# Optimization experiments

Measured on AMD Instinct MI355X. Metric: run time of the kernel, lower is better.

Reference implementation:

```python
import jax, jax.numpy as jnp
import numpy as np

L, D, H, KV, HD, FF, V = 2, 2048, 16, 8, 128, 6144, 32000
B, T = 1, 2048
THETA = 1.0e6
EPS = 1e-6
NEG = -1e30


def _rope_tables():
    inv = 1.0 / (THETA ** (np.arange(0, HD, 2, dtype=np.float32) / HD))
    ang = np.arange(T, dtype=np.float32)[:, None] * inv[None, :]
    ang = np.concatenate([ang, ang], axis=1)  # [T, HD]
    return jnp.asarray(np.cos(ang), jnp.float32), jnp.asarray(np.sin(ang), jnp.float32)


def _rmsnorm(x, scale):
    v = jnp.mean(x * x, axis=-1, keepdims=True)
    return x * jax.lax.rsqrt(v + EPS) * scale


def _rope(x, cos, sin):
    # x: [B, h, T, HD]; rotate-half RoPE with full-dim cos/sin tables
    x1, x2 = x[..., : HD // 2], x[..., HD // 2 :]
    rot = jnp.concatenate([-x2, x1], axis=-1)
    return x * cos[None, None] + rot * sin[None, None]


def setup_inputs() -> dict:
    key = jax.random.key(0)
    ks = jax.random.split(key, 12)
    s = 0.02
    return {
        "token_ids": jax.random.randint(ks[0], (B, T), 0, V),
        "emb": jax.random.normal(ks[1], (V, D), jnp.float32) * s,
        "Wq": jax.random.normal(ks[2], (L, D, H * HD), jnp.float32) * s,
        "Wk": jax.random.normal(ks[3], (L, D, KV * HD), jnp.float32) * s,
        "Wv": jax.random.normal(ks[4], (L, D, KV * HD), jnp.float32) * s,
        "Wo": jax.random.normal(ks[5], (L, H * HD, D), jnp.float32) * s,
        "qn": jnp.ones((L, HD), jnp.float32),
        "kn": jnp.ones((L, HD), jnp.float32),
        "W1": jax.random.normal(ks[6], (L, D, FF), jnp.float32) * s,
        "W2": jax.random.normal(ks[7], (L, D, FF), jnp.float32) * s,
        "W3": jax.random.normal(ks[8], (L, FF, D), jnp.float32) * s,
        "ln1": jnp.ones((L, D), jnp.float32),
        "ln2": jnp.ones((L, D), jnp.float32),
        "lnf": jnp.ones((D,), jnp.float32),
    }


def reference(token_ids, emb, Wq, Wk, Wv, Wo, qn, kn, W1, W2, W3, ln1, ln2, lnf):
    cos, sin = _rope_tables()
    x = emb[token_ids]  # [B, T, D]
    causal = jnp.tril(jnp.ones((T, T), dtype=bool))
    G = H // KV
    scale = 1.0 / np.sqrt(HD)
    for l in range(L):
        # attention block
        h = _rmsnorm(x, ln1[l])
        q = (h @ Wq[l]).reshape(B, T, H, HD).transpose(0, 2, 1, 3)   # [B,H,T,HD]
        k = (h @ Wk[l]).reshape(B, T, KV, HD).transpose(0, 2, 1, 3)  # [B,KV,T,HD]
        v = (h @ Wv[l]).reshape(B, T, KV, HD).transpose(0, 2, 1, 3)
        q = _rmsnorm(q, qn[l])
        k = _rmsnorm(k, kn[l])
        q = _rope(q, cos, sin)
        k = _rope(k, cos, sin)
        qg = q.reshape(B, KV, G, T, HD)
        s_att = jnp.einsum("bgqtd,bgsd->bgqts", qg, k) * scale
        s_att = jnp.where(causal, s_att, NEG)
        a = jax.nn.softmax(s_att, axis=-1)
        o = jnp.einsum("bgqts,bgsd->bgqtd", a, v)
        o = o.reshape(B, H, T, HD).transpose(0, 2, 1, 3).reshape(B, T, H * HD)
        x = x + o @ Wo[l]
        # SwiGLU FFN block
        h = _rmsnorm(x, ln2[l])
        x = x + (jax.nn.silu(h @ W1[l]) * (h @ W2[l])) @ W3[l]
    x = _rmsnorm(x, lnf)
    return x @ emb.T  # tied lm head -> [B, T, V]
```

## Files before the change

kernel.cpp:

```cpp
#include <hip/hip_runtime.h>
#include <math.h>

typedef float f32x4 __attribute__((ext_vector_type(4)));
typedef __bf16 bf16x8 __attribute__((ext_vector_type(8)));
typedef unsigned short u16x8 __attribute__((ext_vector_type(8)));

static constexpr int Dm  = 2048;
static constexpr int Tm  = 2048;
static constexpr int Hm  = 16;
static constexpr int KVm = 8;
static constexpr int HDm = 128;
static constexpr int FFm = 6144;
static constexpr int Vm  = 32000;
static constexpr int QKVN = 4096;

__device__ __forceinline__ float b2f(unsigned short u) {
  unsigned int x = ((unsigned int)u) << 16;
  return __builtin_bit_cast(float, x);
}
__device__ __forceinline__ unsigned short f2b(float f) {
  return __builtin_bit_cast(unsigned short, (__bf16)f);
}
__device__ __forceinline__ f32x4 mfma16x16x32(bf16x8 a, bf16x8 b, f32x4 c) {
  return __builtin_amdgcn_mfma_f32_16x16x32_bf16(a, b, c, 0, 0, 0);
}

__device__ __forceinline__ void gload16(const void* g, void* lds) {
  __builtin_amdgcn_global_load_lds(
      (const __attribute__((address_space(1))) unsigned int*)g,
      (__attribute__((address_space(3))) unsigned int*)lds, 16, 0, 0);
}

__device__ __forceinline__ int xcd_swz(int o, int nwg) {
  int q = nwg >> 3, r8 = nwg & 7;
  int xcd = o & 7, pos = o >> 3;
  return (xcd < r8) ? xcd * (q + 1) + pos : r8 * (q + 1) + (xcd - r8) * q + pos;
}

__global__ void rope_tables_k(float* __restrict__ cosT, float* __restrict__ sinT) {
  int t = blockIdx.x;
  int i = threadIdx.x;
  double inv = pow(1000000.0, -(double)i / 64.0);
  double ang = (double)t * inv;
  cosT[t * 64 + i] = (float)cos(ang);
  sinT[t * 64 + i] = (float)sin(ang);
}

__global__ __launch_bounds__(256) void embed_rms_k(const int* __restrict__ ids,
                                                   const float* __restrict__ emb,
                                                   const float* __restrict__ g,
                                                   float* __restrict__ x,
                                                   unsigned short* __restrict__ y) {
  int t = blockIdx.x;
  int id = ids[t];
  const float* src = emb + (size_t)id * Dm;
  float vals[8];
  float s = 0.f;
#pragma unroll
  for (int i = 0; i < 8; ++i) {
    float vv = src[threadIdx.x + i * 256];
    vals[i] = vv;
    s += vv * vv;
  }
#pragma unroll
  for (int off = 32; off; off >>= 1) s += __shfl_xor(s, off);
  __shared__ float red[4];
  if ((threadIdx.x & 63) == 0) red[threadIdx.x >> 6] = s;
  __syncthreads();
  s = (red[0] + red[1]) + (red[2] + red[3]);
  float r = rsqrtf(s * (1.f / Dm) + 1e-6f);
  float* xr = x + (size_t)t * Dm;
  unsigned short* yr = y + (size_t)t * Dm;
#pragma unroll
  for (int i = 0; i < 8; ++i) {
    int d = threadIdx.x + i * 256;
    xr[d] = vals[i];
    yr[d] = f2b(vals[i] * r * g[d]);
  }
}

__global__ __launch_bounds__(256) void cvt_flat_k(const float* __restrict__ src,
                                                  unsigned short* __restrict__ dst) {
  size_t i = ((size_t)blockIdx.x * 256 + threadIdx.x) * 8;
  f32x4 a = *(const f32x4*)(src + i);
  f32x4 b = *(const f32x4*)(src + i + 4);
  u16x8 o;
  o[0] = f2b(a.x); o[1] = f2b(a.y); o[2] = f2b(a.z); o[3] = f2b(a.w);
  o[4] = f2b(b.x); o[5] = f2b(b.y); o[6] = f2b(b.z); o[7] = f2b(b.w);
  *(u16x8*)(dst + i) = o;
}

__global__ __launch_bounds__(256) void rmsnorm_k(const float* __restrict__ x,
                                                 const float* __restrict__ g,
                                                 unsigned short* __restrict__ y) {
  int t = blockIdx.x;
  const float* xr = x + (size_t)t * Dm;
  float vals[8];
  float s = 0.f;
#pragma unroll
  for (int i = 0; i < 8; ++i) {
    float vv = xr[threadIdx.x + i * 256];
    vals[i] = vv;
    s += vv * vv;
  }
#pragma unroll
  for (int off = 32; off; off >>= 1) s += __shfl_xor(s, off);
  __shared__ float red[4];
  if ((threadIdx.x & 63) == 0) red[threadIdx.x >> 6] = s;
  __syncthreads();
  s = (red[0] + red[1]) + (red[2] + red[3]);
  float r = rsqrtf(s * (1.f / Dm) + 1e-6f);
  unsigned short* yr = y + (size_t)t * Dm;
#pragma unroll
  for (int i = 0; i < 8; ++i) {
    int d = threadIdx.x + i * 256;
    yr[d] = f2b(vals[i] * r * g[d]);
  }
}

__global__ __launch_bounds__(256) void qknorm_rope_k(unsigned short* __restrict__ q,
                                                     const float* __restrict__ nrm,
                                                     const float* __restrict__ cosT,
                                                     const float* __restrict__ sinT,
                                                     int nheads) {
  int gw = (int)((blockIdx.x * blockDim.x + threadIdx.x) >> 6);
  int lane = threadIdx.x & 63;
  int t = gw / nheads, h = gw % nheads;
  unsigned short* row = q + ((size_t)t * nheads + h) * HDm;
  float x1 = b2f(row[lane]);
  float x2 = b2f(row[lane + 64]);
  float s = x1 * x1 + x2 * x2;
#pragma unroll
  for (int off = 32; off; off >>= 1) s += __shfl_xor(s, off);
  float r = rsqrtf(s * (1.f / HDm) + 1e-6f);
  float y1 = x1 * r * nrm[lane];
  float y2 = x2 * r * nrm[lane + 64];
  float c = cosT[t * 64 + lane];
  float sn = sinT[t * 64 + lane];
  row[lane]      = f2b(y1 * c - y2 * sn);
  row[lane + 64] = f2b(y2 * c + y1 * sn);
}

__global__ __launch_bounds__(256) void cvtT_k(const float* __restrict__ W,
                                              unsigned short* __restrict__ Wt,
                                              int K, int N) {
  __shared__ __align__(16) unsigned short tile[64][68];
  const int n0 = blockIdx.x * 64, k0 = blockIdx.y * 64;
  const int tid = threadIdx.x;
#pragma unroll
  for (int i = 0; i < 4; ++i) {
    int e = tid + i * 256;
    int r = e >> 4, c4 = (e & 15) * 4;
    f32x4 v = *(const f32x4*)(W + (size_t)(k0 + r) * N + n0 + c4);
    tile[r][c4 + 0] = f2b(v.x);
    tile[r][c4 + 1] = f2b(v.y);
    tile[r][c4 + 2] = f2b(v.z);
    tile[r][c4 + 3] = f2b(v.w);
  }
  __syncthreads();
#pragma unroll
  for (int i = 0; i < 2; ++i) {
    int e = tid + i * 256;
    int rr = e >> 3, cc = (e & 7) * 8;
    u16x8 o;
#pragma unroll
    for (int j = 0; j < 8; ++j) o[j] = tile[cc + j][rr];
    *(u16x8*)(Wt + (size_t)(n0 + rr) * K + k0 + cc) = o;
  }
}

template <int EPI, bool OUTF32>
__global__ __launch_bounds__(256) void gemm2p_k(const unsigned short* __restrict__ A,
                                                const unsigned short* __restrict__ B,
                                                void* __restrict__ C,
                                                void* __restrict__ C2,
                                                void* __restrict__ C3,
                                                int N, int K, int ld, int cOff) {
  __shared__ __align__(16) unsigned short lds[2][2][128 * 64];
  const int tid = threadIdx.x;
  const int nwg = gridDim.x * gridDim.y;
  const int nid = xcd_swz(blockIdx.x + gridDim.x * blockIdx.y, nwg);
  const int bm = nid % gridDim.x, bn = nid / gridDim.x;
  const int w = tid >> 6, lane = tid & 63;
  const int wm = (w >> 1) * 64, wn = (w & 1) * 64;
  const int lr = lane & 15, hi = lane >> 4;
  const int rowA0 = bm * 128, colB0 = bn * 128;
  const int nk = K >> 6;

  const int srow = lane >> 3;
  const int ulog = (lane & 7) ^ srow;
  const unsigned short* gA = A + (size_t)(rowA0 + w * 32 + srow) * ld + ulog * 8;
  const unsigned short* gB = B + (size_t)(colB0 + w * 32 + srow) * ld + ulog * 8;

  int uu[2];
  uu[0] = ((0 + hi) ^ (lr & 7)) * 8;
  uu[1] = ((4 + hi) ^ (lr & 7)) * 8;

  f32x4 acc[4][4] = {};

  auto stage8 = [&](int buf, int k0) {
    unsigned short* lA = &lds[buf][0][(w * 32) * 64];
    unsigned short* lB = &lds[buf][1][(w * 32) * 64];
#pragma unroll
    for (int i = 0; i < 4; ++i) {
      gload16(gA + (size_t)(i * 8) * ld + k0, lA + i * 8 * 64);
      gload16(gB + (size_t)(i * 8) * ld + k0, lB + i * 8 * 64);
    }
  };

  stage8(0, 0);
  asm volatile("s_waitcnt vmcnt(0)" ::: "memory");
  __builtin_amdgcn_s_barrier();

  for (int kt = 0; kt < nk; ++kt) {
    const int cur = kt & 1;
    if (kt + 1 < nk) stage8(cur ^ 1, (kt + 1) << 6);

    const unsigned short* Ac = &lds[cur][0][0];
    const unsigned short* Bc = &lds[cur][1][0];
    bf16x8 av[4][2], bv[4][2];
#pragma unroll
    for (int m = 0; m < 4; ++m) {
      int rb = (wm + m * 16 + lr) * 64;
#pragma unroll
      for (int ks = 0; ks < 2; ++ks)
        av[m][ks] = *(const bf16x8*)&Ac[rb + uu[ks]];
    }
#pragma unroll
    for (int n = 0; n < 4; ++n) {
      int rb = (wn + n * 16 + lr) * 64;
#pragma unroll
      for (int ks = 0; ks < 2; ++ks)
        bv[n][ks] = *(const bf16x8*)&Bc[rb + uu[ks]];
    }
    __builtin_amdgcn_s_setprio(1);
#pragma unroll
    for (int m = 0; m < 4; ++m)
#pragma unroll
      for (int n = 0; n < 4; ++n)
#pragma unroll
        for (int ks = 0; ks < 2; ++ks)
          acc[m][n] = mfma16x16x32(av[m][ks], bv[n][ks], acc[m][n]);
    __builtin_amdgcn_s_setprio(0);

    asm volatile("s_waitcnt vmcnt(0) lgkmcnt(0)" ::: "memory");
    __builtin_amdgcn_sched_barrier(0);
    __builtin_amdgcn_s_barrier();
  }

  const int r0 = rowA0 + wm + hi * 4;
  const int c0 = wn + lr;
#pragma unroll
  for (int m = 0; m < 4; ++m)
#pragma unroll
    for (int n = 0; n < 4; ++n) {
      const int cc = colB0 + c0 + n * 16;
#pragma unroll
      for (int j = 0; j < 4; ++j) {
        int r = r0 + m * 16 + j;
        if (EPI == 0) {
          size_t idx = (size_t)r * N + cOff + cc;
          if (OUTF32) ((float*)C)[idx] = acc[m][n][j];
          else        ((unsigned short*)C)[idx] = f2b(acc[m][n][j]);
        } else if (EPI == 1) {
          ((float*)C)[(size_t)r * N + cc] += acc[m][n][j];
        } else if (EPI == 2) {
          unsigned short* Cb = (unsigned short*)C;
          size_t idx = (size_t)r * N + cc;
          float gg = b2f(Cb[idx]);
          gg = gg / (1.f + __expf(-gg));
          Cb[idx] = f2b(gg * acc[m][n][j]);
        } else {
          unsigned short v = f2b(acc[m][n][j]);
          if (cc < 2048)      ((unsigned short*)C )[(size_t)r * 2048 + cc] = v;
          else if (cc < 3072) ((unsigned short*)C2)[(size_t)r * 1024 + (cc - 2048)] = v;
          else                ((unsigned short*)C3)[(size_t)r * 1024 + (cc - 3072)] = v;
        }
      }
    }
}

#define LDA256(MH)                                                             \
  _Pragma("unroll") for (int m_ = 0; m_ < 4; ++m_)                             \
  _Pragma("unroll") for (int ks_ = 0; ks_ < 2; ++ks_)                          \
    av[m_][ks_] = *(const bf16x8*)&Ac[aBase + (MH) * 4096 + m_ * 1024 + uu[ks_]];
#define LDB256(NH)                                                             \
  _Pragma("unroll") for (int n_ = 0; n_ < 2; ++n_)                             \
  _Pragma("unroll") for (int ks_ = 0; ks_ < 2; ++ks_)                          \
    bv[n_][ks_] = *(const bf16x8*)&Bc[bBase + (NH) * 2048 + n_ * 1024 + uu[ks_]];
#define MMA256(MH, NH)                                                         \
  __builtin_amdgcn_s_setprio(1);                                               \
  _Pragma("unroll") for (int m_ = 0; m_ < 4; ++m_)                             \
  _Pragma("unroll") for (int n_ = 0; n_ < 2; ++n_)                             \
  _Pragma("unroll") for (int ks_ = 0; ks_ < 2; ++ks_)                          \
    acc[(MH) * 4 + m_][(NH) * 2 + n_] = mfma16x16x32(                          \
        av[m_][ks_], bv[n_][ks_], acc[(MH) * 4 + m_][(NH) * 2 + n_]);          \
  __builtin_amdgcn_s_setprio(0);
#define SYNCV                                                                  \
  asm volatile("s_waitcnt vmcnt(4)" ::: "memory");                             \
  __builtin_amdgcn_s_barrier();                                                \
  asm volatile("s_waitcnt lgkmcnt(0)" ::: "memory");                           \
  __builtin_amdgcn_sched_barrier(0);
#define SYNCNV                                                                 \
  __builtin_amdgcn_s_barrier();                                                \
  asm volatile("s_waitcnt lgkmcnt(0)" ::: "memory");                           \
  __builtin_amdgcn_sched_barrier(0);
#define ENDPH __builtin_amdgcn_s_barrier();

template <int EPI, bool OUTF32>
__global__ __launch_bounds__(512) void gemm256_k(const unsigned short* __restrict__ A,
                                                 const unsigned short* __restrict__ B,
                                                 void* __restrict__ C,
                                                 void* __restrict__ C2,
                                                 void* __restrict__ C3,
                                                 int N, int K, int cOff) {
  __shared__ __align__(16) unsigned short lds[2][2][256 * 64];
  const int tid = threadIdx.x;
  const int nwg = gridDim.x * gridDim.y;
  const int nid = xcd_swz(blockIdx.x + gridDim.x * blockIdx.y, nwg);
  const int bm = nid % gridDim.x, bn = nid / gridDim.x;
  const int w = tid >> 6, lane = tid & 63;
  const int wr = w >> 2, wc = w & 3;
  const int lr = lane & 15, hi = lane >> 4;
  const int rowA0 = bm * 256, colB0 = bn * 256;
  const int nk = K >> 6;

  const int srow = lane >> 3;
  const int ulog = (lane & 7) ^ srow;
  const int eaR = (w < 4) ? w * 16 : 128 + (w - 4) * 16;
  const int laR = eaR + 64;
  const int ebR = (w >> 1) * 64 + (w & 1) * 16;
  const int lbR = ebR + 32;
  const unsigned short* gAt = A + (size_t)rowA0 * K + ulog * 8;
  const unsigned short* gBt = B + (size_t)colB0 * K + ulog * 8;

  int uu[2];
  uu[0] = ((0 + hi) ^ (lr & 7)) * 8;
  uu[1] = ((4 + hi) ^ (lr & 7)) * 8;
  const int aBase = (wr * 128 + lr) * 64;
  const int bBase = (wc * 64 + lr) * 64;

  f32x4 acc[8][4] = {};
  bf16x8 av[4][2], bv[2][2];

  auto stage2 = [&](const unsigned short* g, int rbase, unsigned short* l, int k0) {
    gload16(g + (size_t)(rbase + srow) * K + k0, l + rbase * 64);
    gload16(g + (size_t)(rbase + 8 + srow) * K + k0, l + (rbase + 8) * 64);
  };

  stage2(gAt, eaR, &lds[0][0][0], 0);
  stage2(gBt, ebR, &lds[0][1][0], 0);
  stage2(gBt, lbR, &lds[0][1][0], 0);
  stage2(gAt, laR, &lds[0][0][0], 0);
  asm volatile("s_waitcnt vmcnt(0)" ::: "memory");
  __builtin_amdgcn_s_barrier();

  for (int kt = 0; kt < nk; ++kt) {
    unsigned short* Ac = &lds[kt & 1][0][0];
    unsigned short* Bc = &lds[kt & 1][1][0];
    unsigned short* An = &lds[(kt + 1) & 1][0][0];
    unsigned short* Bn = &lds[(kt + 1) & 1][1][0];
    const int k0n = (kt + 1) << 6;
    const bool more = (kt + 1) < nk;

    LDA256(0) LDB256(0)
    if (more) stage2(gAt, eaR, An, k0n);
    SYNCV MMA256(0, 0) ENDPH
    LDB256(1)
    if (more) stage2(gBt, ebR, Bn, k0n);
    SYNCV MMA256(0, 1) ENDPH
    LDA256(1)
    if (more) stage2(gBt, lbR, Bn, k0n);
    SYNCNV MMA256(1, 1) ENDPH
    LDB256(0)
    if (more) stage2(gAt, laR, An, k0n);
    SYNCV MMA256(1, 0) ENDPH
  }

  const int r0 = rowA0 + wr * 128 + hi * 4;
  const int c0 = colB0 + wc * 64 + lr;
#pragma unroll
  for (int mi = 0; mi < 8; ++mi)
#pragma unroll
    for (int n = 0; n < 4; ++n) {
      const int cc = c0 + n * 16;
#pragma unroll
      for (int j = 0; j < 4; ++j) {
        int r = r0 + mi * 16 + j;
        if (EPI == 0) {
          size_t idx = (size_t)r * N + cOff + cc;
          if (OUTF32) ((float*)C)[idx] = acc[mi][n][j];
          else        ((unsigned short*)C)[idx] = f2b(acc[mi][n][j]);
        } else if (EPI == 2) {
          unsigned short* Cb = (unsigned short*)C;
          size_t idx = (size_t)r * N + cc;
          float gg = b2f(Cb[idx]);
          gg = gg / (1.f + __expf(-gg));
          Cb[idx] = f2b(gg * acc[mi][n][j]);
        } else {
          unsigned short v = f2b(acc[mi][n][j]);
          if (cc < 2048)      ((unsigned short*)C )[(size_t)r * 2048 + cc] = v;
          else if (cc < 3072) ((unsigned short*)C2)[(size_t)r * 1024 + (cc - 2048)] = v;
          else                ((unsigned short*)C3)[(size_t)r * 1024 + (cc - 3072)] = v;
        }
      }
    }
}

__global__ __launch_bounds__(256) void attn_k(const unsigned short* __restrict__ qg,
                                              const unsigned short* __restrict__ kg,
                                              const unsigned short* __restrict__ vg,
                                              unsigned short* __restrict__ og) {
  __shared__ __align__(16) unsigned short Ks[64 * 128];
  __shared__ __align__(16) unsigned short Vt[128 * 72];
  __shared__ __align__(16) unsigned short Pl[4 * 16 * 72];
  const int tid = threadIdx.x;
  const int nid = xcd_swz(blockIdx.x + (blockIdx.y << 5), 512);
  const int u = nid & 63;
  const int h = ((nid >> 6) << 1) | (u >> 5);
  const int qt = (u < 32) ? u : 63 - u;
  const int w = tid >> 6, lane = tid & 63;
  const int lr = lane & 15, hi = lane >> 4;
  const int kvh = h >> 1;

  size_t goff[4]; unsigned kdst[4]; int vr[4], vc[4];
#pragma unroll
  for (int i = 0; i < 4; ++i) {
    int e = tid + i * 256;
    int r = e >> 4, c = (e & 15) * 8;
    goff[i] = ((size_t)r * KVm + kvh) * HDm + c;
    kdst[i] = (unsigned)((r * 256 + c * 2) ^ ((r & 7) << 4));
    vr[i] = r; vc[i] = c;
  }

  const int t0 = qt * 64;
  const int ntk = qt + 1;

  bf16x8 qa[4];
  {
    const unsigned short* qrow = qg + ((size_t)(t0 + w * 16 + lr) * Hm + h) * HDm;
#pragma unroll
    for (int ks = 0; ks < 4; ++ks)
      qa[ks] = __builtin_bit_cast(bf16x8, *(const u16x8*)(qrow + ks * 32 + hi * 8));
  }

  f32x4 oa[8] = {};
  float mj[4], lj[4];
#pragma unroll
  for (int j = 0; j < 4; ++j) { mj[j] = -3.0e38f; lj[j] = 0.f; }

  u16x8 kk[4], vv[4];
#pragma unroll
  for (int i = 0; i < 4; ++i) {
    kk[i] = *(const u16x8*)(kg + goff[i]);
    vv[i] = *(const u16x8*)(vg + goff[i]);
  }

  for (int t = 0; t < ntk; ++t) {
    __syncthreads();
#pragma unroll
    for (int i = 0; i < 4; ++i) {
      *(u16x8*)((char*)Ks + kdst[i]) = kk[i];
#pragma unroll
      for (int j = 0; j < 8; ++j) {
        int d = vc[i] + j;
        Vt[d * 72 + (vr[i] ^ (((d >> 3) & 7) << 3))] = vv[i][j];
      }
    }
    if (t + 1 < ntk) {
      size_t add = (size_t)(t + 1) * 64 * KVm * HDm;
#pragma unroll
      for (int i = 0; i < 4; ++i) {
        kk[i] = *(const u16x8*)(kg + goff[i] + add);
        vv[i] = *(const u16x8*)(vg + goff[i] + add);
      }
    }
    __syncthreads();

    const int s0 = t * 64;
    f32x4 s[4] = {};
#pragma unroll
    for (int ks = 0; ks < 4; ++ks)
#pragma unroll
      for (int nt = 0; nt < 4; ++nt) {
        int krow = nt * 16 + lr;
        int kbyte = (krow * 256 + (ks * 32 + hi * 8) * 2) ^ ((krow & 7) << 4);
        bf16x8 kf = __builtin_bit_cast(bf16x8, *(const u16x8*)((char*)Ks + kbyte));
        s[nt] = mfma16x16x32(qa[ks], kf, s[nt]);
      }

    float p[4][4];
    const bool maskt = (t == ntk - 1);
#pragma unroll
    for (int nt = 0; nt < 4; ++nt)
#pragma unroll
      for (int j = 0; j < 4; ++j) {
        float val = s[nt][j] * 0.08838834764831845f;
        if (maskt && (s0 + nt * 16 + lr) > (t0 + w * 16 + hi * 4 + j)) val = -1e30f;
        p[nt][j] = val;
      }

#pragma unroll
    for (int j = 0; j < 4; ++j) {
      float mx = fmaxf(fmaxf(p[0][j], p[1][j]), fmaxf(p[2][j], p[3][j]));
#pragma unroll
      for (int msk = 1; msk < 16; msk <<= 1) mx = fmaxf(mx, __shfl_xor(mx, msk));
      float mnew = fmaxf(mj[j], mx);
      float alpha = __expf(mj[j] - mnew);
      mj[j] = mnew;
      float sum = 0.f;
#pragma unroll
      for (int nt = 0; nt < 4; ++nt) {
        float e = __expf(p[nt][j] - mnew);
        p[nt][j] = e;
        sum += e;
      }
#pragma unroll
      for (int msk = 1; msk < 16; msk <<= 1) sum += __shfl_xor(sum, msk);
      lj[j] = lj[j] * alpha + sum;
#pragma unroll
      for (int nt2 = 0; nt2 < 8; ++nt2) oa[nt2][j] *= alpha;
    }

#pragma unroll
    for (int nt = 0; nt < 4; ++nt)
#pragma unroll
      for (int j = 0; j < 4; ++j)
        Pl[(w * 16 + hi * 4 + j) * 72 + nt * 16 + lr] = f2b(p[nt][j]);
    __builtin_amdgcn_sched_barrier(0);

    bf16x8 pa[2];
#pragma unroll
    for (int ks2 = 0; ks2 < 2; ++ks2)
      pa[ks2] = __builtin_bit_cast(bf16x8,
                 *(const u16x8*)&Pl[(w * 16 + lr) * 72 + ks2 * 32 + hi * 8]);
#pragma unroll
    for (int nt2 = 0; nt2 < 8; ++nt2)
#pragma unroll
      for (int ks2 = 0; ks2 < 2; ++ks2) {
        int d = nt2 * 16 + lr;
        int kv = ks2 * 32 + hi * 8;
        bf16x8 vf = __builtin_bit_cast(bf16x8,
                     *(const u16x8*)&Vt[d * 72 + (kv ^ (((d >> 3) & 7) << 3))]);
        oa[nt2] = mfma16x16x32(pa[ks2], vf, oa[nt2]);
      }
  }

#pragma unroll
  for (int nt2 = 0; nt2 < 8; ++nt2)
#pragma unroll
    for (int j = 0; j < 4; ++j) {
      int row = t0 + w * 16 + hi * 4 + j;
      int d = nt2 * 16 + lr;
      og[((size_t)row * Hm + h) * HDm + d] = f2b(oa[nt2][j] / lj[j]);
    }
}

extern "C" void kernel_launch(void* const* d_in, const int* in_sizes, int n_in,
                              void* d_out, int out_size, void* d_ws, size_t ws_size,
                              hipStream_t stream) {
  (void)in_sizes; (void)n_in; (void)out_size; (void)ws_size;
  const int*   ids = (const int*)d_in[0];
  const float* emb = (const float*)d_in[1];
  const float* Wq  = (const float*)d_in[2];
  const float* Wk  = (const float*)d_in[3];
  const float* Wv  = (const float*)d_in[4];
  const float* Wo  = (const float*)d_in[5];
  const float* qn  = (const float*)d_in[6];
  const float* kn  = (const float*)d_in[7];
  const float* W1  = (const float*)d_in[8];
  const float* W2  = (const float*)d_in[9];
  const float* W3  = (const float*)d_in[10];
  const float* ln1 = (const float*)d_in[11];
  const float* ln2 = (const float*)d_in[12];
  const float* lnf = (const float*)d_in[13];

  char* p = (char*)d_ws;
  float* xf          = (float*)p;          p += (size_t)Tm * Dm * 4;
  unsigned short* hb = (unsigned short*)p; p += (size_t)Tm * Dm * 2;
  float* cosT        = (float*)p;          p += (size_t)Tm * 64 * 4;
  float* sinT        = (float*)p;          p += (size_t)Tm * 64 * 4;
  unsigned short* qb = (unsigned short*)p; p += (size_t)Tm * Hm * HDm * 2;
  unsigned short* kb = (unsigned short*)p; p += (size_t)Tm * KVm * HDm * 2;
  unsigned short* vb = (unsigned short*)p; p += (size_t)Tm * KVm * HDm * 2;
  unsigned short* ob = (unsigned short*)p; p += (size_t)Tm * Hm * HDm * 2;
  unsigned short* wt = (unsigned short*)p; p += (size_t)Dm * FFm * 2;
  unsigned short* g1 = qb;

  rope_tables_k<<<Tm, 64, 0, stream>>>(cosT, sinT);
  embed_rms_k<<<Tm, 256, 0, stream>>>(ids, emb, ln1, xf, hb);

  for (int l = 0; l < 2; ++l) {
    const float* Wq_l = Wq + (size_t)l * Dm * (Hm * HDm);
    const float* Wk_l = Wk + (size_t)l * Dm * (KVm * HDm);
    const float* Wv_l = Wv + (size_t)l * Dm * (KVm * HDm);
    const float* Wo_l = Wo + (size_t)l * (Hm * HDm) * Dm;
    const float* W1_l = W1 + (size_t)l * Dm * FFm;
    const float* W2_l = W2 + (size_t)l * Dm * FFm;
    const float* W3_l = W3 + (size_t)l * FFm * Dm;

    if (l > 0)
      rmsnorm_k<<<Tm, 256, 0, stream>>>(xf, ln1 + (size_t)l * Dm, hb);

    cvtT_k<<<dim3((Hm * HDm) / 64, Dm / 64), 256, 0, stream>>>(Wq_l, wt, Dm, Hm * HDm);
    cvtT_k<<<dim3((KVm * HDm) / 64, Dm / 64), 256, 0, stream>>>(
        Wk_l, wt + (size_t)2048 * Dm, Dm, KVm * HDm);
    cvtT_k<<<dim3((KVm * HDm) / 64, Dm / 64), 256, 0, stream>>>(
        Wv_l, wt + (size_t)3072 * Dm, Dm, KVm * HDm);
    gemm2p_k<3, false><<<dim3(Tm / 128, QKVN / 128), 256, 0, stream>>>(
        hb, wt, qb, kb, vb, QKVN, Dm, Dm, 0);

    qknorm_rope_k<<<(Tm * Hm) / 4, 256, 0, stream>>>(qb, qn + (size_t)l * HDm, cosT, sinT, Hm);
    qknorm_rope_k<<<(Tm * KVm) / 4, 256, 0, stream>>>(kb, kn + (size_t)l * HDm, cosT, sinT, KVm);

    attn_k<<<dim3(32, 16), 256, 0, stream>>>(qb, kb, vb, ob);

    cvtT_k<<<dim3(Dm / 64, (Hm * HDm) / 64), 256, 0, stream>>>(Wo_l, wt, Hm * HDm, Dm);
    gemm2p_k<1, false><<<dim3(Tm / 128, Dm / 128), 256, 0, stream>>>(
        ob, wt, xf, nullptr, nullptr, Dm, Hm * HDm, Hm * HDm, 0);

    rmsnorm_k<<<Tm, 256, 0, stream>>>(xf, ln2 + (size_t)l * Dm, hb);

    cvtT_k<<<dim3(FFm / 64, Dm / 64), 256, 0, stream>>>(W1_l, wt, Dm, FFm);
    gemm256_k<0, false><<<dim3(Tm / 256, FFm / 256), 512, 0, stream>>>(
        hb, wt, g1, nullptr, nullptr, FFm, Dm, 0);
    cvtT_k<<<dim3(FFm / 64, Dm / 64), 256, 0, stream>>>(W2_l, wt, Dm, FFm);
    gemm256_k<2, false><<<dim3(Tm / 256, FFm / 256), 512, 0, stream>>>(
        hb, wt, g1, nullptr, nullptr, FFm, Dm, 0);
    cvtT_k<<<dim3(Dm / 64, FFm / 64), 256, 0, stream>>>(W3_l, wt, FFm, Dm);
    gemm2p_k<1, false><<<dim3(Tm / 128, Dm / 128), 256, 0, stream>>>(
        g1, wt, xf, nullptr, nullptr, Dm, FFm, FFm, 0);
  }

  rmsnorm_k<<<Tm, 256, 0, stream>>>(xf, lnf, hb);

  unsigned short* embB = qb;
  const int chunks[4] = {8192, 8192, 8192, 7424};
  int off = 0;
  for (int c = 0; c < 4; ++c) {
    const int rows = chunks[c];
    cvt_flat_k<<<rows, 256, 0, stream>>>(emb + (size_t)off * Dm, embB);
    gemm256_k<0, true><<<dim3(Tm / 256, rows / 256), 512, 0, stream>>>(
        hb, embB, d_out, nullptr, nullptr, Vm, Dm, off);
    off += rows;
  }
}
```

Baseline: 1.380 ms.

## Split-K the W3 down-projection GEMM into two partials plus a reduce kernel

The FFN down-projection (K=6144, output 2048x2048) now runs as a split-K GEMM with two K halves along grid z. Each half writes fp32 partials to extra workspace, and a new reduce kernel adds both into the residual. The aim is to double the workgroup count (256 to 512 tiles) so the GPU's CUs stay busy on this long-K GEMM. The cost is extra partial-buffer traffic and one more launch, and the path runs only when the workspace is large enough.

```diff
diff --git a/kernel.cpp b/kernel.cpp
--- a/kernel.cpp
+++ b/kernel.cpp
@@ -88,6 +88,17 @@
   o[0] = f2b(a.x); o[1] = f2b(a.y); o[2] = f2b(a.z); o[3] = f2b(a.w);
   o[4] = f2b(b.x); o[5] = f2b(b.y); o[6] = f2b(b.z); o[7] = f2b(b.w);
   *(u16x8*)(dst + i) = o;
+}
+
+__global__ __launch_bounds__(256) void reduce2_k(const float* __restrict__ p0,
+                                                 const float* __restrict__ p1,
+                                                 float* __restrict__ x) {
+  size_t i = ((size_t)blockIdx.x * 256 + threadIdx.x) * 4;
+  f32x4 a = *(const f32x4*)(p0 + i);
+  f32x4 b = *(const f32x4*)(p1 + i);
+  f32x4 c = *(const f32x4*)(x + i);
+  c.x += a.x + b.x; c.y += a.y + b.y; c.z += a.z + b.z; c.w += a.w + b.w;
+  *(f32x4*)(x + i) = c;
 }
 
 __global__ __launch_bounds__(256) void rmsnorm_k(const float* __restrict__ x,
@@ -186,11 +197,12 @@
   const int lr = lane & 15, hi = lane >> 4;
   const int rowA0 = bm * 128, colB0 = bn * 128;
   const int nk = K >> 6;
+  const int kz = blockIdx.z * K;
 
   const int srow = lane >> 3;
   const int ulog = (lane & 7) ^ srow;
-  const unsigned short* gA = A + (size_t)(rowA0 + w * 32 + srow) * ld + ulog * 8;
-  const unsigned short* gB = B + (size_t)(colB0 + w * 32 + srow) * ld + ulog * 8;
+  const unsigned short* gA = A + (size_t)(rowA0 + w * 32 + srow) * ld + kz + ulog * 8;
+  const unsigned short* gB = B + (size_t)(colB0 + w * 32 + srow) * ld + kz + ulog * 8;
 
   int uu[2];
   uu[0] = ((0 + hi) ^ (lr & 7)) * 8;
@@ -270,6 +282,9 @@
           float gg = b2f(Cb[idx]);
           gg = gg / (1.f + __expf(-gg));
           Cb[idx] = f2b(gg * acc[m][n][j]);
+        } else if (EPI == 5) {
+          float* Cz = (float*)C + (size_t)blockIdx.z * gridDim.x * 128 * N;
+          Cz[(size_t)r * N + cc] = acc[m][n][j];
         } else {
           unsigned short v = f2b(acc[m][n][j]);
           if (cc < 2048)      ((unsigned short*)C )[(size_t)r * 2048 + cc] = v;
@@ -559,7 +574,7 @@
 extern "C" void kernel_launch(void* const* d_in, const int* in_sizes, int n_in,
                               void* d_out, int out_size, void* d_ws, size_t ws_size,
                               hipStream_t stream) {
-  (void)in_sizes; (void)n_in; (void)out_size; (void)ws_size;
+  (void)in_sizes; (void)n_in; (void)out_size;
   const int*   ids = (const int*)d_in[0];
   const float* emb = (const float*)d_in[1];
   const float* Wq  = (const float*)d_in[2];
@@ -587,6 +602,10 @@
   unsigned short* wt = (unsigned short*)p; p += (size_t)Dm * FFm * 2;
   unsigned short* g1 = qb;
 
+  const size_t extOff = (size_t)(p - (char*)d_ws);
+  float* pp = (float*)p;
+  const bool haveP = ws_size >= extOff + (size_t)2 * Tm * Dm * 4;
+
   rope_tables_k<<<Tm, 64, 0, stream>>>(cosT, sinT);
   embed_rms_k<<<Tm, 256, 0, stream>>>(ids, emb, ln1, xf, hb);
 
@@ -628,8 +647,15 @@
     gemm256_k<2, false><<<dim3(Tm / 256, FFm / 256), 512, 0, stream>>>(
         hb, wt, g1, nullptr, nullptr, FFm, Dm, 0);
     cvtT_k<<<dim3(Dm / 64, FFm / 64), 256, 0, stream>>>(W3_l, wt, FFm, Dm);
-    gemm2p_k<1, false><<<dim3(Tm / 128, Dm / 128), 256, 0, stream>>>(
-        g1, wt, xf, nullptr, nullptr, Dm, FFm, FFm, 0);
+    if (haveP) {
+      gemm2p_k<5, true><<<dim3(Tm / 128, Dm / 128, 2), 256, 0, stream>>>(
+          g1, wt, pp, nullptr, nullptr, Dm, FFm / 2, FFm, 0);
+      reduce2_k<<<(Tm * Dm) / 1024, 256, 0, stream>>>(
+          pp, pp + (size_t)Tm * Dm, xf);
+    } else {
+      gemm2p_k<1, false><<<dim3(Tm / 128, Dm / 128), 256, 0, stream>>>(
+          g1, wt, xf, nullptr, nullptr, Dm, FFm, FFm, 0);
+    }
   }
 
   rmsnorm_k<<<Tm, 256, 0, stream>>>(xf, lnf, hb);
```

New measurement: 1.377 ms, median of 2. About the same (-0.2%).
